# Performance work log

Measured on AMD Instinct MI355X. Metric: run time of the kernel, lower is better.

The kernel has to match this reference:

```python
import jax, jax.numpy as jnp
import numpy as np
from jax import lax

EPS = 1e-5      # InstanceNorm2d default eps
SLOPE = 0.2     # LeakyReLU negative slope
K = 3           # kernel size
PAD = 1


def _conv(x, w, pad=PAD):
    # x: [B,C,H,W], w: [O,I,K,K], stride 1
    return lax.conv_general_dilated(x, w, (1, 1), [(pad, pad), (pad, pad)],
                                    dimension_numbers=('NCHW', 'OIHW', 'NCHW'))


def _instance_norm(x, gamma, beta):
    mu = jnp.mean(x, (2, 3), keepdims=True)
    var = jnp.mean((x - mu) ** 2, (2, 3), keepdims=True)
    xn = (x - mu) * lax.rsqrt(var + EPS)
    return xn * gamma[None, :, None, None] + beta[None, :, None, None]


def _lrelu(x):
    return jnp.where(x >= 0, x, SLOPE * x)


def _deform_conv(x, w_off, b_off, w_def):
    # DCNv2: offsets+mask predicted by a 3x3 conv, then modulated bilinear sampling.
    B, C, H, W = x.shape
    om = _conv(x, w_off) + b_off[None, :, None, None]       # [B, 3*K*K, H, W]
    o1, o2, m = jnp.split(om, 3, axis=1)                    # each [B, K*K, H, W]
    off = jnp.concatenate([o1, o2], axis=1)                 # [B, 2*K*K, H, W]
    dy = off[:, 0::2]                                       # [B, K*K, H, W] y-offsets
    dx = off[:, 1::2]                                       # [B, K*K, H, W] x-offsets
    mask = jax.nn.sigmoid(m)                                # [B, K*K, H, W]

    ky = jnp.repeat(jnp.arange(K), K).astype(x.dtype)       # tap row index per k
    kx = jnp.tile(jnp.arange(K), K).astype(x.dtype)         # tap col index per k
    py = dy + jnp.arange(H, dtype=x.dtype)[None, None, :, None] - PAD + ky[None, :, None, None]
    px = dx + jnp.arange(W, dtype=x.dtype)[None, None, None, :] - PAD + kx[None, :, None, None]

    y0 = jnp.floor(py); x0 = jnp.floor(px)
    ly = py - y0; lx = px - x0
    y0i = y0.astype(jnp.int32); x0i = x0.astype(jnp.int32)

    xf = x.reshape(B, C, H * W)

    def gather(iy, ix):
        valid = ((iy >= 0) & (iy < H) & (ix >= 0) & (ix < W)).astype(x.dtype)
        idx = jnp.clip(iy, 0, H - 1) * W + jnp.clip(ix, 0, W - 1)
        v = jax.vmap(lambda f, i: jnp.take(f, i, axis=-1))(xf, idx)  # [B,C,K*K,H,W]
        return v * valid[:, None]

    samp = (gather(y0i, x0i)         * ((1 - ly) * (1 - lx))[:, None]
          + gather(y0i, x0i + 1)     * ((1 - ly) * lx)[:, None]
          + gather(y0i + 1, x0i)     * (ly * (1 - lx))[:, None]
          + gather(y0i + 1, x0i + 1) * (ly * lx)[:, None])          # [B,C,K*K,H,W]

    wk = w_def.reshape(w_def.shape[0], C, K * K)            # [O,C,K*K]
    return jnp.einsum('ock,bckhw,bkhw->bohw', wk, samp, mask)


def setup_inputs() -> dict:
    key = jax.random.key(0)
    ks = jax.random.split(key, 10)
    B, C, H, W = 4, 128, 96, 96
    x = jax.random.normal(ks[0], (B, C, H, W), jnp.float32)
    g1 = 1.0 + 0.05 * jax.random.normal(ks[1], (C,), jnp.float32)
    b1 = 0.05 * jax.random.normal(ks[2], (C,), jnp.float32)
    g2 = 1.0 + 0.05 * jax.random.normal(ks[3], (C,), jnp.float32)
    b2 = 0.05 * jax.random.normal(ks[4], (C,), jnp.float32)
    w1 = jax.random.normal(ks[5], (C, C, K, K), jnp.float32) * 0.03
    bc1 = 0.01 * jax.random.normal(ks[6], (C,), jnp.float32)
    # offset/mask conv: zero-init in the original; use small random values so the
    # irregular bilinear-sampling path is actually exercised.
    w_off = jax.random.normal(ks[7], (3 * K * K, C, K, K), jnp.float32) * 0.01
    b_off = 0.01 * jax.random.normal(ks[8], (3 * K * K,), jnp.float32)
    w_def = jax.random.normal(ks[9], (C, C, K, K), jnp.float32) * 0.03  # DeformConv has bias=None
    return {"x": x, "g1": g1, "b1": b1, "g2": g2, "b2": b2,
            "w1": w1, "bc1": bc1, "w_off": w_off, "b_off": b_off, "w_def": w_def}


def reference(x, g1, b1, g2, b2, w1, bc1, w_off, b_off, w_def):
    h = _lrelu(_instance_norm(x, g1, b1))
    h = _conv(h, w1) + bc1[None, :, None, None]
    h = _lrelu(_instance_norm(h, g2, b2))
    h = _deform_conv(h, w_off, b_off, w_def)
    return h + x
```

## Files before the change

### kernel.cpp

```cpp
#include <hip/hip_runtime.h>
#include <hip/hip_fp16.h>
#include <math.h>

#define HWN 9216
#define HD 96
#define WD 96

typedef _Float16 h8v __attribute__((ext_vector_type(8)));
typedef float f16x16 __attribute__((ext_vector_type(16)));

__device__ __forceinline__ ushort f2h(float f) {
  return __half_as_ushort(__float2half(f));
}
__device__ __forceinline__ __half2 u2h(unsigned u) {
  return __builtin_bit_cast(__half2, u);
}
__device__ __forceinline__ unsigned h2u(__half2 h) {
  return __builtin_bit_cast(unsigned, h);
}
__device__ __forceinline__ h8v u4h(uint4 v) {
  return __builtin_bit_cast(h8v, v);
}
__device__ __forceinline__ f16x16 mfma32(h8v a, h8v b, f16x16 c) {
  return __builtin_amdgcn_mfma_f32_32x32x16_f16(a, b, c, 0, 0, 0);
}
__device__ __forceinline__ __half2 pkmax2(__half2 a, __half2 b) {
  unsigned r;
  asm("v_pk_max_f16 %0, %1, %2" : "=v"(r) : "v"(h2u(a)), "v"(h2u(b)));
  return u2h(r);
}
__device__ __forceinline__ __half2 lrelu2(__half2 v, __half2 c02) {
  return pkmax2(v, __hmul2(v, c02));
}

__global__ __launch_bounds__(256) void packxt_kernel(
    const float* __restrict__ w1, const float* __restrict__ wdef,
    const float* __restrict__ woff, const float* __restrict__ x,
    ushort* __restrict__ w1p, ushort* __restrict__ wdp, ushort* __restrict__ wofp,
    unsigned* __restrict__ xh, float* __restrict__ partS, float* __restrict__ partQ) {
  __shared__ float tl[128][97];
  int bid = blockIdx.x;
  int t = threadIdx.x;
  if (bid < 162) {
    int i = bid * 256 + t;
    const float* src;
    ushort* dst;
    int CT, CO_real, fi;
    if (i < 18432) { src = w1; dst = w1p; CT = 4; CO_real = 128; fi = i; }
    else if (i < 36864) { src = wdef; dst = wdp; CT = 4; CO_real = 128; fi = i - 18432; }
    else { src = woff; dst = wofp; CT = 1; CO_real = 27; fi = i - 36864; }
    int lane = fi & 63;
    int j = fi >> 6;
    int ks = j & 7; j >>= 3;
    int ct = j % CT;
    int kk = j / CT;
    int co = ct * 32 + (lane & 31);
    int c0 = ks * 16 + (lane >> 5) * 8;
    ushort fr[8];
#pragma unroll
    for (int e = 0; e < 8; ++e) {
      float v = 0.f;
      if (co < CO_real) v = src[(size_t)(co * 128 + c0 + e) * 9 + kk];
      fr[e] = f2h(v);
    }
    uint4 o4;
    o4.x = (unsigned)fr[0] | ((unsigned)fr[1] << 16);
    o4.y = (unsigned)fr[2] | ((unsigned)fr[3] << 16);
    o4.z = (unsigned)fr[4] | ((unsigned)fr[5] << 16);
    o4.w = (unsigned)fr[6] | ((unsigned)fr[7] << 16);
    *(uint4*)(dst + (size_t)fi * 8) = o4;
    return;
  }
  int xb = bid - 162;
  int b = xb / 96, y = xb % 96;
  const float* sbase = x + (size_t)b * 128 * HWN + y * WD;
  for (int i = t; i < 12288; i += 256) {
    int c = i / 96, xx = i - c * 96;
    tl[c][xx] = sbase[(size_t)c * HWN + xx];
  }
  __syncthreads();
  {
    int c = t >> 1, half = t & 1;
    float S = 0.f, Q = 0.f;
    for (int j = 0; j < 48; ++j) {
      float v = tl[c][half * 48 + j];
      S += v;
      Q += v * v;
    }
    S += __shfl_xor(S, 1, 64);
    Q += __shfl_xor(Q, 1, 64);
    if (half == 0) {
      partS[((size_t)(b * 96 + y)) * 128 + c] = S;
      partQ[((size_t)(b * 96 + y)) * 128 + c] = Q;
    }
  }
  unsigned* dbase = xh + (size_t)(b * 96 + y) * 96 * 64;
  for (int i = t; i < 6144; i += 256) {
    int xx = i >> 6, c2 = i & 63;
    unsigned lo = f2h(tl[2 * c2][xx]);
    unsigned hi = f2h(tl[2 * c2 + 1][xx]);
    dbase[xx * 64 + c2] = lo | (hi << 16);
  }
}

__global__ __launch_bounds__(64) void finalize_kernel(
    const float* __restrict__ partS, const float* __restrict__ partQ,
    const float* __restrict__ gamma, const float* __restrict__ beta,
    float* __restrict__ sa_, float* __restrict__ sb_, int ntiles) {
  int bc = blockIdx.x;
  int b = bc >> 7, c = bc & 127;
  float S = 0.f, Q = 0.f;
  for (int tl = threadIdx.x; tl < ntiles; tl += 64) {
    S += partS[((size_t)b * ntiles + tl) * 128 + c];
    Q += partQ[((size_t)b * ntiles + tl) * 128 + c];
  }
#pragma unroll
  for (int off = 32; off > 0; off >>= 1) {
    S += __shfl_down(S, off, 64);
    Q += __shfl_down(Q, off, 64);
  }
  if (threadIdx.x == 0) {
    float mu = S / (float)HWN;
    float var = Q / (float)HWN - mu * mu;
    float rs = rsqrtf(var + 1e-5f);
    float a = rs * gamma[c];
    sa_[bc] = a;
    sb_[bc] = beta[c] - mu * a;
  }
}

__global__ __launch_bounds__(256) void stats2_kernel(
    const ushort* __restrict__ hBh, float* __restrict__ partS,
    float* __restrict__ partQ) {
  int tile = blockIdx.x;
  int b = blockIdx.y;
  int t = threadIdx.x;
  int cc = t & 15, pp = t >> 4;
  int wid = t >> 6, lane = t & 63;
  const ushort* base = hBh + ((size_t)b * HWN + tile * 144) * 128 + cc * 8;
  float S[8], Q[8];
#pragma unroll
  for (int e = 0; e < 8; ++e) { S[e] = 0.f; Q[e] = 0.f; }
  for (int i = 0; i < 9; ++i) {
    int pix = i * 16 + pp;
    uint4 v = *(const uint4*)(base + (size_t)pix * 128);
    unsigned ar[4] = {v.x, v.y, v.z, v.w};
#pragma unroll
    for (int j = 0; j < 4; ++j) {
      float2 f = __half22float2(u2h(ar[j]));
      S[2 * j] += f.x; Q[2 * j] += f.x * f.x;
      S[2 * j + 1] += f.y; Q[2 * j + 1] += f.y * f.y;
    }
  }
#pragma unroll
  for (int e = 0; e < 8; ++e) {
    S[e] += __shfl_xor(S[e], 16, 64); Q[e] += __shfl_xor(Q[e], 16, 64);
    S[e] += __shfl_xor(S[e], 32, 64); Q[e] += __shfl_xor(Q[e], 32, 64);
  }
  __shared__ float red[2][4][16][8];
  if (lane < 16) {
#pragma unroll
    for (int e = 0; e < 8; ++e) { red[0][wid][lane][e] = S[e]; red[1][wid][lane][e] = Q[e]; }
  }
  __syncthreads();
  if (t < 16) {
#pragma unroll
    for (int e = 0; e < 8; ++e) {
      float s = red[0][0][t][e] + red[0][1][t][e] + red[0][2][t][e] + red[0][3][t][e];
      float q = red[1][0][t][e] + red[1][1][t][e] + red[1][2][t][e] + red[1][3][t][e];
      partS[((size_t)b * 64 + tile) * 128 + t * 8 + e] = s;
      partQ[((size_t)b * 64 + tile) * 128 + t * 8 + e] = q;
    }
  }
}

__global__ __launch_bounds__(512) void conv1_mfma(
    const ushort* __restrict__ inp, const float* __restrict__ sa_,
    const float* __restrict__ sb_, const ushort* __restrict__ wp,
    const float* __restrict__ bias, ushort* __restrict__ outh) {
  __shared__ ushort halo[100 * 128];
  __shared__ __half2 sah[64], sbh[64];
  int b = blockIdx.y;
  int tile = blockIdx.x;
  int Y0 = (tile / 12) * 8, X0 = (tile % 12) * 8;
  int t = threadIdx.x;
  int lane = t & 63, w = t >> 6;
  if (t < 64) {
    sah[t] = __floats2half2_rn(sa_[b * 128 + 2 * t], sa_[b * 128 + 2 * t + 1]);
    sbh[t] = __floats2half2_rn(sb_[b * 128 + 2 * t], sb_[b * 128 + 2 * t + 1]);
  }
  __syncthreads();
  const __half2 c02 = __float2half2_rn(0.2f);
  const ushort* ib = inp + (size_t)b * HWN * 128;
  for (int i = t; i < 400; i += 512) {
    int r = i >> 2, q = i & 3;
    int gy = Y0 - 1 + r / 10, gx = X0 - 1 + r % 10;
    bool inb = ((unsigned)gy < 96u) && ((unsigned)gx < 96u);
    const uint4* gp4 = (const uint4*)(ib + (size_t)(gy * 96 + gx) * 128 + q * 32);
#pragma unroll
    for (int cc = 0; cc < 4; ++cc) {
      uint4 v = make_uint4(0, 0, 0, 0);
      if (inb) {
        uint4 g = gp4[cc];
        unsigned ar[4] = {g.x, g.y, g.z, g.w};
        int c2b = (q * 4 + cc) * 4;
#pragma unroll
        for (int j = 0; j < 4; ++j) {
          __half2 hv = __hfma2(u2h(ar[j]), sah[c2b + j], sbh[c2b + j]);
          hv = lrelu2(hv, c02);
          ar[j] = h2u(hv);
        }
        v.x = ar[0]; v.y = ar[1]; v.z = ar[2]; v.w = ar[3];
      }
      int ch = (q * 4 + cc) ^ (r & 7);
      *(uint4*)&halo[r * 128 + ch * 8] = v;
    }
  }
  __syncthreads();

  int ct = w >> 1, pt = w & 1;
  int pl = lane & 31, kh = lane >> 5;
  int p = pt * 32 + pl;
  f16x16 acc = (f16x16)(0.f);

  uint4 Acur[8], Anxt[8];
#pragma unroll
  for (int ks = 0; ks < 8; ++ks)
    Acur[ks] = *(const uint4*)(wp + (size_t)((0 * 4 + ct) * 8 + ks) * 512 + lane * 8);

  for (int kk = 0; kk < 9; ++kk) {
    if (kk < 8) {
#pragma unroll
      for (int ks = 0; ks < 8; ++ks)
        Anxt[ks] = *(const uint4*)(wp + (size_t)(((kk + 1) * 4 + ct) * 8 + ks) * 512 + lane * 8);
    }
    int ky = kk / 3, kx = kk % 3;
    int r = ((p >> 3) + ky) * 10 + (p & 7) + kx;
    __builtin_amdgcn_s_setprio(1);
#pragma unroll
    for (int ks = 0; ks < 8; ++ks) {
      int u = (ks * 2 + kh) ^ (r & 7);
      h8v bf = *(const h8v*)&halo[r * 128 + u * 8];
      acc = mfma32(u4h(Acur[ks]), bf, acc);
    }
    __builtin_amdgcn_s_setprio(0);
    if (kk < 8) {
#pragma unroll
      for (int ks = 0; ks < 8; ++ks) Acur[ks] = Anxt[ks];
    }
  }
  int gp = (Y0 + (p >> 3)) * 96 + X0 + (p & 7);
#pragma unroll
  for (int g = 0; g < 4; ++g) {
    int ch0 = ct * 32 + 4 * kh + 8 * g;
    float v0 = acc[4 * g + 0] + bias[ch0 + 0];
    float v1 = acc[4 * g + 1] + bias[ch0 + 1];
    float v2 = acc[4 * g + 2] + bias[ch0 + 2];
    float v3 = acc[4 * g + 3] + bias[ch0 + 3];
    uint2 o;
    o.x = (unsigned)f2h(v0) | ((unsigned)f2h(v1) << 16);
    o.y = (unsigned)f2h(v2) | ((unsigned)f2h(v3) << 16);
    *(uint2*)&outh[((size_t)b * HWN + gp) * 128 + ch0] = o;
  }
}

__device__ __forceinline__ uint4 gaffine(const ushort* hb, int pix, int cc,
                                         const __half2* sa2v, const __half2* sb2v,
                                         __half2 c02) {
  uint4 g = *(const uint4*)(hb + (size_t)pix * 128 + cc * 8);
  unsigned ar[4] = {g.x, g.y, g.z, g.w};
#pragma unroll
  for (int j = 0; j < 4; ++j) {
    __half2 hv = __hfma2(u2h(ar[j]), sa2v[j], sb2v[j]);
    hv = lrelu2(hv, c02);
    ar[j] = h2u(hv);
  }
  return make_uint4(ar[0], ar[1], ar[2], ar[3]);
}

__global__ __launch_bounds__(256) void deform_fused(
    const ushort* __restrict__ h2n, const float* __restrict__ sa_,
    const float* __restrict__ sb_, const ushort* __restrict__ wofp,
    const float* __restrict__ boff, const ushort* __restrict__ wdp,
    const float* __restrict__ x, float* __restrict__ out) {
  __shared__ __align__(16) ushort halo[96 * 128];
  __shared__ __align__(16) ushort S[32 * 128];
  __shared__ __align__(16) ushort4 idxs[9][32];
  __shared__ __align__(16) ushort4 wgtc[9][32];
  __shared__ __half2 sah[64], sbh[64];
  float* om_t = (float*)S;
  int bid = blockIdx.x;
  int swz = (bid & 7) * 144 + (bid >> 3);
  int b = swz / 288;
  int tile = swz % 288;
  int Y0 = (tile / 12) * 4, X0 = (tile % 12) * 8;
  int t = threadIdx.x;
  int lane = t & 63, w = t >> 6;
  const ushort* hb = h2n + (size_t)b * HWN * 128;
  if (t < 64) {
    sah[t] = __floats2half2_rn(sa_[b * 128 + 2 * t], sa_[b * 128 + 2 * t + 1]);
    sbh[t] = __floats2half2_rn(sb_[b * 128 + 2 * t], sb_[b * 128 + 2 * t + 1]);
  }
  __syncthreads();
  const __half2 c02 = __float2half2_rn(0.2f);

  for (int i = t; i < 1536; i += 256) {
    int pix = i >> 4, u = i & 15;
    int gy = Y0 - 2 + pix / 12, gx = X0 - 2 + pix % 12;
    uint4 v = make_uint4(0, 0, 0, 0);
    if (((unsigned)gy < 96u) && ((unsigned)gx < 96u)) {
      uint4 g = *(const uint4*)(hb + (size_t)(gy * 96 + gx) * 128 + u * 8);
      unsigned ar[4] = {g.x, g.y, g.z, g.w};
#pragma unroll
      for (int j = 0; j < 4; ++j) {
        __half2 hv = __hfma2(u2h(ar[j]), sah[u * 4 + j], sbh[u * 4 + j]);
        hv = lrelu2(hv, c02);
        ar[j] = h2u(hv);
      }
      v.x = ar[0]; v.y = ar[1]; v.z = ar[2]; v.w = ar[3];
    }
    *(uint4*)&halo[pix * 128 + ((u ^ (pix & 15)) * 8)] = v;
  }
  __syncthreads();

  if (w == 0) {
    int pl = lane & 31, kh = lane >> 5;
    int p = pl;
    f16x16 accm = (f16x16)(0.f);
    uint4 Ac[8], An[8];
#pragma unroll
    for (int ks = 0; ks < 8; ++ks)
      Ac[ks] = *(const uint4*)(wofp + (size_t)(0 * 8 + ks) * 512 + lane * 8);
    for (int kk = 0; kk < 9; ++kk) {
      if (kk < 8) {
#pragma unroll
        for (int ks = 0; ks < 8; ++ks)
          An[ks] = *(const uint4*)(wofp + (size_t)((kk + 1) * 8 + ks) * 512 + lane * 8);
      }
      int ky = kk / 3, kx = kk % 3;
      int hp = (1 + (p >> 3) + ky) * 12 + 1 + (p & 7) + kx;
#pragma unroll
      for (int ks = 0; ks < 8; ++ks) {
        int u = (ks * 2 + kh) ^ (hp & 15);
        h8v bf = *(const h8v*)&halo[hp * 128 + u * 8];
        accm = mfma32(u4h(Ac[ks]), bf, accm);
      }
      if (kk < 8) {
#pragma unroll
        for (int ks = 0; ks < 8; ++ks) Ac[ks] = An[ks];
      }
    }
#pragma unroll
    for (int reg = 0; reg < 16; ++reg) {
      int co = 4 * kh + (reg & 3) + 8 * (reg >> 2);
      if (co < 27) om_t[co * 32 + p] = accm[reg] + boff[co];
    }
  }
  __syncthreads();

  for (int i = t; i < 288; i += 256) {
    int k = i >> 5, p = i & 31;
    int yy = Y0 + (p >> 3), xx = X0 + (p & 7);
    float dy = om_t[(2 * k) * 32 + p];
    float dx = om_t[(2 * k + 1) * 32 + p];
    float mv = om_t[(18 + k) * 32 + p];
    float mask = 1.0f / (1.0f + expf(-mv));
    float py = dy + (float)(yy - 1 + (k / 3));
    float px = dx + (float)(xx - 1 + (k % 3));
    float fy = floorf(py), fx = floorf(px);
    float lyf = py - fy, lxf = px - fx;
    int y0 = (int)fy, x0 = (int)fx;
    int y1 = y0 + 1, x1 = x0 + 1;
    bool vy0 = (y0 >= 0) && (y0 < HD);
    bool vy1 = (y1 >= 0) && (y1 < HD);
    bool vx0 = (x0 >= 0) && (x0 < WD);
    bool vx1 = (x1 >= 0) && (x1 < WD);
    int y0c = min(max(y0, 0), HD - 1), y1c = min(max(y1, 0), HD - 1);
    int x0c = min(max(x0, 0), WD - 1), x1c = min(max(x1, 0), WD - 1);
    float w0 = (1.f - lyf) * (1.f - lxf) * ((vy0 && vx0) ? mask : 0.f);
    float w1v = (1.f - lyf) * lxf * ((vy0 && vx1) ? mask : 0.f);
    float w2 = lyf * (1.f - lxf) * ((vy1 && vx0) ? mask : 0.f);
    float w3 = lyf * lxf * ((vy1 && vx1) ? mask : 0.f);
    bool inh = (y0c >= Y0 - 2) && (y1c <= Y0 + 5) && (x0c >= X0 - 2) && (x1c <= X0 + 9);
    ushort4 sidx;
    if (inh) {
      int sy0 = y0c - (Y0 - 2), sy1 = y1c - (Y0 - 2);
      int sx0 = x0c - (X0 - 2), sx1 = x1c - (X0 - 2);
      sidx.x = (ushort)(sy0 * 12 + sx0);
      sidx.y = (ushort)(sy0 * 12 + sx1);
      sidx.z = (ushort)(sy1 * 12 + sx0);
      sidx.w = (ushort)(sy1 * 12 + sx1);
    } else {
      sidx.x = (ushort)((y0c * WD + x0c) | 0x8000);
      sidx.y = (ushort)(y0c * WD + x1c);
      sidx.z = (ushort)(y1c * WD + x0c);
      sidx.w = (ushort)(y1c * WD + x1c);
    }
    idxs[k][p] = sidx;
    ushort4 wc;
    wc.x = f2h(w0); wc.y = f2h(w1v); wc.z = f2h(w2); wc.w = f2h(w3);
    wgtc[k][p] = wc;
  }
  __syncthreads();

  int cc = t & 15;
  int pp = t >> 4;
  int ct = w;
  int pl = lane & 31, kh = lane >> 5;
  int pg = pl;
  f16x16 acc = (f16x16)(0.f);
  __half2 sa2v[4], sb2v[4];
#pragma unroll
  for (int j = 0; j < 4; ++j) { sa2v[j] = sah[cc * 4 + j]; sb2v[j] = sbh[cc * 4 + j]; }

  int gp = (Y0 + (pg >> 3)) * 96 + X0 + (pg & 7);
  float xr[16];
#pragma unroll
  for (int reg = 0; reg < 16; ++reg) {
    int co = ct * 32 + 4 * kh + (reg & 3) + 8 * (reg >> 2);
    xr[reg] = x[(size_t)(b * 128 + co) * HWN + gp];
  }

  uint4 AW[8];
  for (int k = 0; k < 9; ++k) {
    const ushort* wk = wdp + (size_t)k * 16384;
#pragma unroll
    for (int ks = 0; ks < 8; ++ks)
      AW[ks] = *(const uint4*)(wk + (size_t)(ct * 8 + ks) * 512 + lane * 8);
#pragma unroll
    for (int i2 = 0; i2 < 2; ++i2) {
      int p = pp + 16 * i2;
      ushort4 sidx = idxs[k][p];
      ushort4 wc = wgtc[k][p];
      uint4 C0, C1, C2, C3;
      if (sidx.x & 0x8000u) {
        C0 = gaffine(hb, sidx.x & 0x7fff, cc, sa2v, sb2v, c02);
        C1 = gaffine(hb, sidx.y, cc, sa2v, sb2v, c02);
        C2 = gaffine(hb, sidx.z, cc, sa2v, sb2v, c02);
        C3 = gaffine(hb, sidx.w, cc, sa2v, sb2v, c02);
      } else {
        C0 = *(const uint4*)&halo[sidx.x * 128 + ((cc ^ (sidx.x & 15)) * 8)];
        C1 = *(const uint4*)&halo[sidx.y * 128 + ((cc ^ (sidx.y & 15)) * 8)];
        C2 = *(const uint4*)&halo[sidx.z * 128 + ((cc ^ (sidx.z & 15)) * 8)];
        C3 = *(const uint4*)&halo[sidx.w * 128 + ((cc ^ (sidx.w & 15)) * 8)];
      }
      __half2 a0 = u2h((unsigned)wc.x * 0x10001u);
      __half2 a1 = u2h((unsigned)wc.y * 0x10001u);
      __half2 a2 = u2h((unsigned)wc.z * 0x10001u);
      __half2 a3 = u2h((unsigned)wc.w * 0x10001u);
      __half2 s0 = __hmul2(u2h(C0.x), a0);
      __half2 s1 = __hmul2(u2h(C0.y), a0);
      __half2 s2 = __hmul2(u2h(C0.z), a0);
      __half2 s3 = __hmul2(u2h(C0.w), a0);
      s0 = __hfma2(u2h(C1.x), a1, s0); s1 = __hfma2(u2h(C1.y), a1, s1);
      s2 = __hfma2(u2h(C1.z), a1, s2); s3 = __hfma2(u2h(C1.w), a1, s3);
      s0 = __hfma2(u2h(C2.x), a2, s0); s1 = __hfma2(u2h(C2.y), a2, s1);
      s2 = __hfma2(u2h(C2.z), a2, s2); s3 = __hfma2(u2h(C2.w), a2, s3);
      s0 = __hfma2(u2h(C3.x), a3, s0); s1 = __hfma2(u2h(C3.y), a3, s1);
      s2 = __hfma2(u2h(C3.z), a3, s2); s3 = __hfma2(u2h(C3.w), a3, s3);
      uint4 o4;
      o4.x = h2u(s0); o4.y = h2u(s1); o4.z = h2u(s2); o4.w = h2u(s3);
      *(uint4*)&S[p * 128 + ((cc ^ (p & 15)) * 8)] = o4;
    }
    asm volatile("s_waitcnt lgkmcnt(0)" ::: "memory");
    __builtin_amdgcn_s_barrier();
    __builtin_amdgcn_s_setprio(1);
#pragma unroll
    for (int ks = 0; ks < 8; ++ks) {
      int u = (ks * 2 + kh) ^ (pg & 15);
      h8v bf = *(const h8v*)&S[pg * 128 + u * 8];
      acc = mfma32(u4h(AW[ks]), bf, acc);
    }
    __builtin_amdgcn_s_setprio(0);
    asm volatile("s_waitcnt lgkmcnt(0)" ::: "memory");
    __builtin_amdgcn_s_barrier();
  }
#pragma unroll
  for (int reg = 0; reg < 16; ++reg) {
    int co = ct * 32 + 4 * kh + (reg & 3) + 8 * (reg >> 2);
    size_t oi = (size_t)(b * 128 + co) * HWN + gp;
    out[oi] = acc[reg] + xr[reg];
  }
}

extern "C" void kernel_launch(void* const* d_in, const int* in_sizes, int n_in,
                              void* d_out, int out_size, void* d_ws, size_t ws_size,
                              hipStream_t stream) {
  const float* x = (const float*)d_in[0];
  const float* g1 = (const float*)d_in[1];
  const float* b1 = (const float*)d_in[2];
  const float* g2 = (const float*)d_in[3];
  const float* b2 = (const float*)d_in[4];
  const float* w1 = (const float*)d_in[5];
  const float* bc1 = (const float*)d_in[6];
  const float* w_off = (const float*)d_in[7];
  const float* b_off = (const float*)d_in[8];
  const float* w_def = (const float*)d_in[9];
  float* out = (float*)d_out;
  float* ws = (float*)d_ws;

  ushort* w1p = (ushort*)ws;
  ushort* wofp = (ushort*)(ws + 73728);
  ushort* wdp = (ushort*)(ws + 92160);
  float* sa1 = ws + 165888;
  float* sb1 = ws + 166400;
  float* sa2 = ws + 166912;
  float* sb2 = ws + 167424;
  float* partS1 = ws + 167936;
  float* partQ1 = ws + 217088;
  float* partS2 = ws + 266240;
  float* partQ2 = ws + 299008;
  ushort* xh = (ushort*)(ws + 331776);
  ushort* hBh = (ushort*)(ws + 2691072);

  packxt_kernel<<<546, 256, 0, stream>>>(w1, w_def, w_off, x, w1p, wdp, wofp,
                                         (unsigned*)xh, partS1, partQ1);
  finalize_kernel<<<512, 64, 0, stream>>>(partS1, partQ1, g1, b1, sa1, sb1, 96);
  conv1_mfma<<<dim3(144, 4), 512, 0, stream>>>(xh, sa1, sb1, w1p, bc1, hBh);
  stats2_kernel<<<dim3(64, 4), 256, 0, stream>>>(hBh, partS2, partQ2);
  finalize_kernel<<<512, 64, 0, stream>>>(partS2, partQ2, g2, b2, sa2, sb2, 64);
  deform_fused<<<dim3(1152), 256, 0, stream>>>(hBh, sa2, sb2, wofp, b_off, wdp, x, out);
}
```

Baseline: 83.12 us.

## Split offset conv across all waves and double-buffer deform staging tile

The offset/mask convolution previously ran on wave 0 alone while the other three waves sat idle. It now spreads the nine kernel taps across all four waves. Each wave writes its partial sums to shared memory, and the sampling stage adds the partials together with the bias. The deform-conv staging buffer S is now double-buffered by tap parity, which removes the second barrier in each tap iteration. The cost is more shared memory, plus weight loads that are no longer prefetched in the offset conv.

```diff
diff --git a/kernel.cpp b/kernel.cpp
--- a/kernel.cpp
+++ b/kernel.cpp
@@ -284,11 +284,11 @@
     const float* __restrict__ boff, const ushort* __restrict__ wdp,
     const float* __restrict__ x, float* __restrict__ out) {
   __shared__ __align__(16) ushort halo[96 * 128];
-  __shared__ __align__(16) ushort S[32 * 128];
+  __shared__ __align__(16) ushort S[2][32 * 128];
   __shared__ __align__(16) ushort4 idxs[9][32];
   __shared__ __align__(16) ushort4 wgtc[9][32];
   __shared__ __half2 sah[64], sbh[64];
-  float* om_t = (float*)S;
+  float* pf = (float*)S;
   int bid = blockIdx.x;
   int swz = (bid & 7) * 144 + (bid >> 3);
   int b = swz / 288;
@@ -323,37 +323,25 @@
   }
   __syncthreads();
 
-  if (w == 0) {
+  {
     int pl = lane & 31, kh = lane >> 5;
     int p = pl;
     f16x16 accm = (f16x16)(0.f);
-    uint4 Ac[8], An[8];
-#pragma unroll
-    for (int ks = 0; ks < 8; ++ks)
-      Ac[ks] = *(const uint4*)(wofp + (size_t)(0 * 8 + ks) * 512 + lane * 8);
-    for (int kk = 0; kk < 9; ++kk) {
-      if (kk < 8) {
-#pragma unroll
-        for (int ks = 0; ks < 8; ++ks)
-          An[ks] = *(const uint4*)(wofp + (size_t)((kk + 1) * 8 + ks) * 512 + lane * 8);
-      }
+    for (int kk = w; kk < 9; kk += 4) {
       int ky = kk / 3, kx = kk % 3;
       int hp = (1 + (p >> 3) + ky) * 12 + 1 + (p & 7) + kx;
 #pragma unroll
       for (int ks = 0; ks < 8; ++ks) {
+        uint4 a = *(const uint4*)(wofp + (size_t)(kk * 8 + ks) * 512 + lane * 8);
         int u = (ks * 2 + kh) ^ (hp & 15);
         h8v bf = *(const h8v*)&halo[hp * 128 + u * 8];
-        accm = mfma32(u4h(Ac[ks]), bf, accm);
-      }
-      if (kk < 8) {
-#pragma unroll
-        for (int ks = 0; ks < 8; ++ks) Ac[ks] = An[ks];
+        accm = mfma32(u4h(a), bf, accm);
       }
     }
 #pragma unroll
     for (int reg = 0; reg < 16; ++reg) {
       int co = 4 * kh + (reg & 3) + 8 * (reg >> 2);
-      if (co < 27) om_t[co * 32 + p] = accm[reg] + boff[co];
+      pf[(w * 32 + co) * 32 + p] = accm[reg];
     }
   }
   __syncthreads();
@@ -361,9 +349,13 @@
   for (int i = t; i < 288; i += 256) {
     int k = i >> 5, p = i & 31;
     int yy = Y0 + (p >> 3), xx = X0 + (p & 7);
-    float dy = om_t[(2 * k) * 32 + p];
-    float dx = om_t[(2 * k + 1) * 32 + p];
-    float mv = om_t[(18 + k) * 32 + p];
+    int cdy = 2 * k, cdx = 2 * k + 1, cm = 18 + k;
+    float dy = pf[(0 * 32 + cdy) * 32 + p] + pf[(1 * 32 + cdy) * 32 + p] +
+               pf[(2 * 32 + cdy) * 32 + p] + pf[(3 * 32 + cdy) * 32 + p] + boff[cdy];
+    float dx = pf[(0 * 32 + cdx) * 32 + p] + pf[(1 * 32 + cdx) * 32 + p] +
+               pf[(2 * 32 + cdx) * 32 + p] + pf[(3 * 32 + cdx) * 32 + p] + boff[cdx];
+    float mv = pf[(0 * 32 + cm) * 32 + p] + pf[(1 * 32 + cm) * 32 + p] +
+               pf[(2 * 32 + cm) * 32 + p] + pf[(3 * 32 + cm) * 32 + p] + boff[cm];
     float mask = 1.0f / (1.0f + expf(-mv));
     float py = dy + (float)(yy - 1 + (k / 3));
     float px = dx + (float)(xx - 1 + (k % 3));
@@ -427,6 +419,7 @@
 #pragma unroll
     for (int ks = 0; ks < 8; ++ks)
       AW[ks] = *(const uint4*)(wk + (size_t)(ct * 8 + ks) * 512 + lane * 8);
+    ushort* Sb_w = S[k & 1];
 #pragma unroll
     for (int i2 = 0; i2 < 2; ++i2) {
       int p = pp + 16 * i2;
@@ -460,20 +453,19 @@
       s2 = __hfma2(u2h(C3.z), a3, s2); s3 = __hfma2(u2h(C3.w), a3, s3);
       uint4 o4;
       o4.x = h2u(s0); o4.y = h2u(s1); o4.z = h2u(s2); o4.w = h2u(s3);
-      *(uint4*)&S[p * 128 + ((cc ^ (p & 15)) * 8)] = o4;
+      *(uint4*)&Sb_w[p * 128 + ((cc ^ (p & 15)) * 8)] = o4;
     }
     asm volatile("s_waitcnt lgkmcnt(0)" ::: "memory");
     __builtin_amdgcn_s_barrier();
+    const ushort* Sb = S[k & 1];
     __builtin_amdgcn_s_setprio(1);
 #pragma unroll
     for (int ks = 0; ks < 8; ++ks) {
       int u = (ks * 2 + kh) ^ (pg & 15);
-      h8v bf = *(const h8v*)&S[pg * 128 + u * 8];
+      h8v bf = *(const h8v*)&Sb[pg * 128 + u * 8];
       acc = mfma32(u4h(AW[ks]), bf, acc);
     }
     __builtin_amdgcn_s_setprio(0);
-    asm volatile("s_waitcnt lgkmcnt(0)" ::: "memory");
-    __builtin_amdgcn_s_barrier();
   }
 #pragma unroll
   for (int reg = 0; reg < 16; ++reg) {
```

Result: no change. 81.90 us (-1.5%).
